# Optimization experiments

Hardware: AMD Instinct MI355X
Metric: run time of the kernel (lower is better)

The kernel has to match this reference:

```python
import jax, jax.numpy as jnp
import numpy as np

B, M, N, DIM, P, Q, OUT = 64, 64, 64, 3, 3, 3, 512


def gen_knot_vector(p, n):
    # p leading zeros + linspace(0,1,n-p) + p trailing ones (repo convention)
    return np.concatenate([np.zeros(p), np.linspace(0.0, 1.0, n - p), np.ones(p)])


def precompute_basis(n_ctrl, p, out_dim):
    """Knot spans and Cox-de Boor basis values (Piegl A2.1/A2.2) on a uniform param grid."""
    U = gen_knot_vector(p, n_ctrl)
    u = np.linspace(0.0, 1.0, out_dim)
    # largest i with U[i] <= u, clamped to the valid span range [p, n_ctrl-2]
    spans = np.clip(np.searchsorted(U, u, side='right') - 1, p, n_ctrl - 2)
    Nmat = np.zeros((out_dim, p + 1))
    for i in range(out_dim):
        s, uu = int(spans[i]), u[i]
        Ni = np.zeros(p + 1); Ni[0] = 1.0
        left = np.zeros(p + 1); right = np.zeros(p + 1)
        for j in range(1, p + 1):
            left[j] = uu - U[s + 1 - j]
            right[j] = U[s + j] - uu
            saved = 0.0
            for r in range(j):
                temp = Ni[r] / (right[r + 1] + left[j - r])
                Ni[r] = saved + right[r + 1] * temp
                saved = left[j - r] * temp
            Ni[j] = saved
        Nmat[i] = Ni
    # gather index table: control-point row span-p+l for l in 0..p
    idx = spans[:, None] - p + np.arange(p + 1)[None, :]
    return Nmat.astype(np.float32), idx.astype(np.int64)


def setup_inputs() -> dict:
    key = jax.random.key(0)
    k1, k2 = jax.random.split(key)
    xyz = jax.random.normal(k1, (B, M, N, DIM), dtype=jnp.float32)
    w = jax.random.uniform(k2, (B, M, N, 1), dtype=jnp.float32, minval=0.5, maxval=1.5)
    ctrl = jnp.concatenate([xyz, w], axis=-1)  # homogeneous control points [B,M,N,4]
    Nu, iu = precompute_basis(M, P, OUT)
    Nv, iv = precompute_basis(N, Q, OUT)
    return {"ctrl": ctrl, "Nu": jnp.asarray(Nu), "Nv": jnp.asarray(Nv),
            "iu": jnp.asarray(iu), "iv": jnp.asarray(iv)}


def reference(ctrl, Nu, Nv, iu, iv):
    D = ctrl.shape[-1] - 1
    U_, V_ = Nu.shape[0], Nv.shape[0]
    surf = jnp.zeros((ctrl.shape[0], U_, V_, ctrl.shape[-1]), dtype=ctrl.dtype)
    for l in range(iu.shape[1]):          # p+1 terms (fixed, small)
        rows = ctrl[:, iu[:, l]]          # [B, U, N, D+1]
        for r in range(iv.shape[1]):      # q+1 terms (fixed, small)
            pts = rows[:, :, iv[:, r]]    # [B, U, V, D+1]
            w = Nu[:, l][:, None] * Nv[None, :, r]  # [U, V]
            surf = surf + w[None, :, :, None] * pts
    return surf[..., :D] / surf[..., D:]  # perspective divide
```

## Files before the change

kernel.cpp:

```cpp
#include <hip/hip_runtime.h>


#define OUTDIM 512
#define CTRL_N 64
#define TU 8

__global__ __launch_bounds__(256) void surf_eval_kernel(
    const float* __restrict__ ctrl,
    const float* __restrict__ Nu,
    const float* __restrict__ Nv,
    const int*   __restrict__ iu,
    const int*   __restrict__ iv,
    float*       __restrict__ out)
{
    __shared__ float4 rows[TU * CTRL_N];
    __shared__ __align__(16) float stg[2][OUTDIM * 3];

    const int blk = blockIdx.x;
    const int b  = blk >> 6;
    const int U0 = (blk & 63) * TU;
    const int t  = threadIdx.x;

    {
        const int u  = t >> 5;
        const int n0 = t & 31;
        const int U  = U0 + u;
        const float4 nu  = *(const float4*)(Nu + U * 4);
        const int4   iu4 = *(const int4*)(iu + U * 4);
        const float* cb = ctrl + (size_t)b * (64 * 64 * 4);
        const float* r0 = cb + (size_t)iu4.x * (CTRL_N * 4);
        const float* r1 = cb + (size_t)iu4.y * (CTRL_N * 4);
        const float* r2 = cb + (size_t)iu4.z * (CTRL_N * 4);
        const float* r3 = cb + (size_t)iu4.w * (CTRL_N * 4);

#pragma unroll
        for (int k = 0; k < 2; ++k) {
            const int n = n0 + 32 * k;
            const float4 p0 = *(const float4*)(r0 + n * 4);
            const float4 p1 = *(const float4*)(r1 + n * 4);
            const float4 p2 = *(const float4*)(r2 + n * 4);
            const float4 p3 = *(const float4*)(r3 + n * 4);
            float4 acc;
            acc.x = nu.x * p0.x + nu.y * p1.x + nu.z * p2.x + nu.w * p3.x;
            acc.y = nu.x * p0.y + nu.y * p1.y + nu.z * p2.y + nu.w * p3.y;
            acc.z = nu.x * p0.z + nu.y * p1.z + nu.z * p2.z + nu.w * p3.z;
            acc.w = nu.x * p0.w + nu.y * p1.w + nu.z * p2.w + nu.w * p3.w;
            rows[u * CTRL_N + n] = acc;
        }
    }
    __syncthreads();

    const int v0 = t << 1;
    const float4 nvA = *(const float4*)(Nv + v0 * 4);
    const float4 nvB = *(const float4*)(Nv + v0 * 4 + 4);
    const int    iA  = iv[v0 * 4];
    const int    dB  = iv[v0 * 4 + 4] - iA;

    const float wB0 = dB ? 0.0f  : nvB.x;
    const float wB1 = dB ? nvB.x : nvB.y;
    const float wB2 = dB ? nvB.y : nvB.z;
    const float wB3 = dB ? nvB.z : nvB.w;
    const float wB4 = dB ? nvB.w : 0.0f;

    float* orow = out + ((size_t)b * OUTDIM + U0) * (OUTDIM * 3);

    auto compute_and_stage = [&](int u) {
        const float4* ru = rows + u * CTRL_N;
        const float4 q0 = ru[iA + 0];
        const float4 q1 = ru[iA + 1];
        const float4 q2 = ru[iA + 2];
        const float4 q3 = ru[iA + 3];
        const float4 q4 = ru[iA + 4];

        float sxA = nvA.x * q0.x + nvA.y * q1.x + nvA.z * q2.x + nvA.w * q3.x;
        float syA = nvA.x * q0.y + nvA.y * q1.y + nvA.z * q2.y + nvA.w * q3.y;
        float szA = nvA.x * q0.z + nvA.y * q1.z + nvA.z * q2.z + nvA.w * q3.z;
        float swA = nvA.x * q0.w + nvA.y * q1.w + nvA.z * q2.w + nvA.w * q3.w;

        float sxB = wB0 * q0.x + wB1 * q1.x + wB2 * q2.x + wB3 * q3.x + wB4 * q4.x;
        float syB = wB0 * q0.y + wB1 * q1.y + wB2 * q2.y + wB3 * q3.y + wB4 * q4.y;
        float szB = wB0 * q0.z + wB1 * q1.z + wB2 * q2.z + wB3 * q3.z + wB4 * q4.z;
        float swB = wB0 * q0.w + wB1 * q1.w + wB2 * q2.w + wB3 * q3.w + wB4 * q4.w;

        const float invA = __builtin_amdgcn_rcpf(swA);
        const float invB = __builtin_amdgcn_rcpf(swB);

        float2* sp = (float2*)&stg[u & 1][6 * t];
        sp[0] = make_float2(sxA * invA, syA * invA);
        sp[1] = make_float2(szA * invA, sxB * invB);
        sp[2] = make_float2(syB * invB, szB * invB);
    };

    compute_and_stage(0);

#pragma unroll
    for (int u = 0; u < TU; ++u) {
        __syncthreads();
        if (u + 1 < TU) compute_and_stage(u + 1);

        const float4* sb = (const float4*)stg[u & 1];
        float* og = orow + u * (OUTDIM * 3);
        *(float4*)(og + 4 * t) = sb[t];
        if (t < 128)
            *(float4*)(og + 4 * (256 + t)) = sb[256 + t];
    }
}

extern "C" void kernel_launch(void* const* d_in, const int* in_sizes, int n_in,
                              void* d_out, int out_size, void* d_ws, size_t ws_size,
                              hipStream_t stream) {
    const float* ctrl = (const float*)d_in[0];
    const float* Nu   = (const float*)d_in[1];
    const float* Nv   = (const float*)d_in[2];
    const int*   iu   = (const int*)d_in[3];
    const int*   iv   = (const int*)d_in[4];
    float* out = (float*)d_out;

    const int nblocks = 64 * (OUTDIM / TU);
    surf_eval_kernel<<<nblocks, 256, 0, stream>>>(ctrl, Nu, Nv, iu, iv, out);
}
```

Measured before the change: 206.0 us.

## Drop LDS output staging and store directly; split row buffer into float2 arrays

Removes the double-buffered shared-memory staging of output rows and its per-row barriers. Each thread now writes its six output floats straight to global memory as three float2 stores. The intermediate row buffer is split into separate xy and zw float2 arrays, which changes the LDS access pattern and footprint. Direct stores are 8-byte strided per thread instead of fully coalesced 16-byte writes, which could reduce store efficiency, in exchange for fewer synchronizations and less LDS traffic.

```diff
diff --git a/kernel.cpp b/kernel.cpp
--- a/kernel.cpp
+++ b/kernel.cpp
@@ -13,8 +13,8 @@
     const int*   __restrict__ iv,
     float*       __restrict__ out)
 {
-    __shared__ float4 rows[TU * CTRL_N];
-    __shared__ __align__(16) float stg[2][OUTDIM * 3];
+    __shared__ float2 pxy[TU * CTRL_N];
+    __shared__ float2 pzw[TU * CTRL_N];
 
     const int blk = blockIdx.x;
     const int b  = blk >> 6;
@@ -45,7 +45,8 @@
             acc.y = nu.x * p0.y + nu.y * p1.y + nu.z * p2.y + nu.w * p3.y;
             acc.z = nu.x * p0.z + nu.y * p1.z + nu.z * p2.z + nu.w * p3.z;
             acc.w = nu.x * p0.w + nu.y * p1.w + nu.z * p2.w + nu.w * p3.w;
-            rows[u * CTRL_N + n] = acc;
+            pxy[u * CTRL_N + n] = make_float2(acc.x, acc.y);
+            pzw[u * CTRL_N + n] = make_float2(acc.z, acc.w);
         }
     }
     __syncthreads();
@@ -62,47 +63,40 @@
     const float wB3 = dB ? nvB.z : nvB.w;
     const float wB4 = dB ? nvB.w : 0.0f;
 
-    float* orow = out + ((size_t)b * OUTDIM + U0) * (OUTDIM * 3);
+    const size_t obase = ((size_t)b * OUTDIM + U0) * OUTDIM;
 
-    auto compute_and_stage = [&](int u) {
-        const float4* ru = rows + u * CTRL_N;
-        const float4 q0 = ru[iA + 0];
-        const float4 q1 = ru[iA + 1];
-        const float4 q2 = ru[iA + 2];
-        const float4 q3 = ru[iA + 3];
-        const float4 q4 = ru[iA + 4];
+#pragma unroll
+    for (int u = 0; u < TU; ++u) {
+        const float2* uxy = pxy + u * CTRL_N + iA;
+        const float2* uzw = pzw + u * CTRL_N + iA;
+        const float2 xy0 = uxy[0];
+        const float2 xy1 = uxy[1];
+        const float2 xy2 = uxy[2];
+        const float2 xy3 = uxy[3];
+        const float2 xy4 = uxy[4];
+        const float2 zw0 = uzw[0];
+        const float2 zw1 = uzw[1];
+        const float2 zw2 = uzw[2];
+        const float2 zw3 = uzw[3];
+        const float2 zw4 = uzw[4];
 
-        float sxA = nvA.x * q0.x + nvA.y * q1.x + nvA.z * q2.x + nvA.w * q3.x;
-        float syA = nvA.x * q0.y + nvA.y * q1.y + nvA.z * q2.y + nvA.w * q3.y;
-        float szA = nvA.x * q0.z + nvA.y * q1.z + nvA.z * q2.z + nvA.w * q3.z;
-        float swA = nvA.x * q0.w + nvA.y * q1.w + nvA.z * q2.w + nvA.w * q3.w;
+        const float sxA = nvA.x * xy0.x + nvA.y * xy1.x + nvA.z * xy2.x + nvA.w * xy3.x;
+        const float syA = nvA.x * xy0.y + nvA.y * xy1.y + nvA.z * xy2.y + nvA.w * xy3.y;
+        const float szA = nvA.x * zw0.x + nvA.y * zw1.x + nvA.z * zw2.x + nvA.w * zw3.x;
+        const float swA = nvA.x * zw0.y + nvA.y * zw1.y + nvA.z * zw2.y + nvA.w * zw3.y;
 
-        float sxB = wB0 * q0.x + wB1 * q1.x + wB2 * q2.x + wB3 * q3.x + wB4 * q4.x;
-        float syB = wB0 * q0.y + wB1 * q1.y + wB2 * q2.y + wB3 * q3.y + wB4 * q4.y;
-        float szB = wB0 * q0.z + wB1 * q1.z + wB2 * q2.z + wB3 * q3.z + wB4 * q4.z;
-        float swB = wB0 * q0.w + wB1 * q1.w + wB2 * q2.w + wB3 * q3.w + wB4 * q4.w;
+        const float sxB = wB0 * xy0.x + wB1 * xy1.x + wB2 * xy2.x + wB3 * xy3.x + wB4 * xy4.x;
+        const float syB = wB0 * xy0.y + wB1 * xy1.y + wB2 * xy2.y + wB3 * xy3.y + wB4 * xy4.y;
+        const float szB = wB0 * zw0.x + wB1 * zw1.x + wB2 * zw2.x + wB3 * zw3.x + wB4 * zw4.x;
+        const float swB = wB0 * zw0.y + wB1 * zw1.y + wB2 * zw2.y + wB3 * zw3.y + wB4 * zw4.y;
 
         const float invA = __builtin_amdgcn_rcpf(swA);
         const float invB = __builtin_amdgcn_rcpf(swB);
 
-        float2* sp = (float2*)&stg[u & 1][6 * t];
-        sp[0] = make_float2(sxA * invA, syA * invA);
-        sp[1] = make_float2(szA * invA, sxB * invB);
-        sp[2] = make_float2(syB * invB, szB * invB);
-    };
-
-    compute_and_stage(0);
-
-#pragma unroll
-    for (int u = 0; u < TU; ++u) {
-        __syncthreads();
-        if (u + 1 < TU) compute_and_stage(u + 1);
-
-        const float4* sb = (const float4*)stg[u & 1];
-        float* og = orow + u * (OUTDIM * 3);
-        *(float4*)(og + 4 * t) = sb[t];
-        if (t < 128)
-            *(float4*)(og + 4 * (256 + t)) = sb[256 + t];
+        float* og = out + (obase + (size_t)u * OUTDIM + v0) * 3;
+        *(float2*)(og + 0) = make_float2(sxA * invA, syA * invA);
+        *(float2*)(og + 2) = make_float2(szA * invA, sxB * invB);
+        *(float2*)(og + 4) = make_float2(syB * invB, szB * invB);
     }
 }
 
```

Result: slower. 212.6 us (+3.2%).
